# Kernel tuning notes

Hardware: AMD Instinct MI355X
Metric: run time of the kernel (lower is better)

The kernel has to match this reference:

```python
import math
import jax, jax.numpy as jnp
import numpy as np

DIM = 4096
N_HEADS = 32
N_KV_HEADS = 8
HEAD_DIM = DIM // N_HEADS          # 128
N_REP = N_HEADS // N_KV_HEADS      # 4
BATCH = 2
SEQLEN = 2048
MAX_BATCH = 2
MAX_SEQ = 2048
THETA = 10000.0


def _precompute_freqs(dim, end, theta=THETA):
    freqs = 1.0 / theta ** (np.arange(0, dim, 2)[: dim // 2].astype(np.float32) / dim)
    t = np.arange(end, dtype=np.float32)
    ang = np.outer(t, freqs)  # [end, dim//2]
    return jnp.asarray(np.cos(ang), jnp.float32), jnp.asarray(np.sin(ang), jnp.float32)


def setup_inputs() -> dict:
    key = jax.random.key(0)
    ks = jax.random.split(key, 6)
    x = jax.random.normal(ks[0], (BATCH, SEQLEN, DIM), jnp.float32)
    scale = 0.02
    wq = jax.random.normal(ks[1], (DIM, N_HEADS * HEAD_DIM), jnp.float32) * scale
    wk = jax.random.normal(ks[2], (DIM, N_KV_HEADS * HEAD_DIM), jnp.float32) * scale
    wv = jax.random.normal(ks[3], (DIM, N_KV_HEADS * HEAD_DIM), jnp.float32) * scale
    wo = jax.random.normal(ks[4], (N_HEADS * HEAD_DIM, DIM), jnp.float32) * scale
    cache_k = jnp.zeros((MAX_BATCH, MAX_SEQ, N_KV_HEADS, HEAD_DIM), jnp.float32)
    cache_v = jnp.zeros((MAX_BATCH, MAX_SEQ, N_KV_HEADS, HEAD_DIM), jnp.float32)
    freqs_cos, freqs_sin = _precompute_freqs(HEAD_DIM, SEQLEN)
    # additive causal mask, [S, S]
    mask = jnp.where(jnp.tril(jnp.ones((SEQLEN, SEQLEN), bool)), 0.0, -1e9).astype(jnp.float32)
    return {"x": x, "wq": wq, "wk": wk, "wv": wv, "wo": wo,
            "cache_k": cache_k, "cache_v": cache_v,
            "freqs_cos": freqs_cos, "freqs_sin": freqs_sin,
            "mask": mask, "start_pos": 0}


def _apply_rotary(t, cos, sin):
    # t: [B, S, H, D]; cos/sin: [S, D/2] -> broadcast [1, S, 1, D/2]
    B, S, H, D = t.shape
    tr = t.reshape(B, S, H, D // 2, 2)
    re, im = tr[..., 0], tr[..., 1]
    c = cos[None, :, None, :]
    s = sin[None, :, None, :]
    out = jnp.stack([re * c - im * s, re * s + im * c], axis=-1)
    return out.reshape(B, S, H, D)


def reference(x, wq, wk, wv, wo, cache_k, cache_v, freqs_cos, freqs_sin, mask, start_pos):
    B, S, D = x.shape
    xq = (x @ wq).reshape(B, S, N_HEADS, HEAD_DIM)
    xk = (x @ wk).reshape(B, S, N_KV_HEADS, HEAD_DIM)
    xv = (x @ wv).reshape(B, S, N_KV_HEADS, HEAD_DIM)
    xq = _apply_rotary(xq, freqs_cos, freqs_sin)
    xk = _apply_rotary(xk, freqs_cos, freqs_sin)
    # KV-cache write (start_pos is a static Python int)
    ck = cache_k.at[:B, start_pos:start_pos + S].set(xk)
    cv = cache_v.at[:B, start_pos:start_pos + S].set(xv)
    keys = ck[:B, :start_pos + S]    # [B, T, KVH, D]
    values = cv[:B, :start_pos + S]
    # GQA: repeat kv heads
    keys = jnp.repeat(keys, N_REP, axis=2)      # [B, T, H, D]
    values = jnp.repeat(values, N_REP, axis=2)
    scores = jnp.einsum('bqhd,bkhd->bhqk', xq, keys) / math.sqrt(HEAD_DIM)
    scores = scores + mask[None, None, :, :]
    probs = jax.nn.softmax(scores.astype(jnp.float32), axis=-1).astype(xq.dtype)
    out = jnp.einsum('bhqk,bkhd->bqhd', probs, values).reshape(B, S, N_HEADS * HEAD_DIM)
    return out @ wo
```

## Files before the change

### kernel.cpp

```cpp
#include <hip/hip_runtime.h>
#include <stdint.h>

typedef __attribute__((ext_vector_type(4))) float f32x4;
typedef __attribute__((ext_vector_type(4))) unsigned short u16x4;
typedef __attribute__((ext_vector_type(8))) unsigned short u16x8;
typedef __attribute__((ext_vector_type(8))) short s16x8;

#define NH   32
#define NKV  8
#define HD   128
#define SEQ  2048
#define MTOK 4096

__device__ __forceinline__ float b2f(unsigned short u) {
  union { float f; unsigned int i; } v; v.i = ((unsigned int)u) << 16; return v.f;
}
__device__ __forceinline__ unsigned short f2b(float f) {
  unsigned int i = __float_as_uint(f);
  return (unsigned short)((i + 0x7fffu + ((i >> 16) & 1u)) >> 16);
}

__global__ void convert_f32_bf16(const float* __restrict__ in,
                                 unsigned short* __restrict__ out, int n4) {
  int i = blockIdx.x * 256 + threadIdx.x;
  if (i >= n4) return;
  f32x4 v = *(const f32x4*)(in + (size_t)i * 4);
  u16x4 r;
  r.x = f2b(v.x); r.y = f2b(v.y); r.z = f2b(v.z); r.w = f2b(v.w);
  *(u16x4*)(out + (size_t)i * 4) = r;
}

__global__ void tconv(const float* __restrict__ W, unsigned short* __restrict__ WT, int N) {
  __shared__ float tile[32][33];
  int k0 = blockIdx.x * 32, n0 = blockIdx.y * 32;
  int t = threadIdx.x;
  int r = t >> 3;
  int c = (t & 7) * 4;
  f32x4 v = *(const f32x4*)&W[(size_t)(k0 + r) * N + n0 + c];
  tile[r][c + 0] = v.x; tile[r][c + 1] = v.y; tile[r][c + 2] = v.z; tile[r][c + 3] = v.w;
  __syncthreads();
  u16x4 o;
  o.x = f2b(tile[c + 0][r]); o.y = f2b(tile[c + 1][r]);
  o.z = f2b(tile[c + 2][r]); o.w = f2b(tile[c + 3][r]);
  *(u16x4*)&WT[(size_t)(n0 + r) * 4096 + k0 + c] = o;
}

__global__ void vtrans(const unsigned short* __restrict__ vb, unsigned short* __restrict__ vtb) {
  __shared__ unsigned short tile[32][36];
  int s0 = blockIdx.x * 32, d0 = blockIdx.y * 32;
  int bkv = blockIdx.z; int b = bkv >> 3, kvh = bkv & 7;
  int t = threadIdx.x;
  int r = t >> 3, c = (t & 7) * 4;
  u16x4 v = *(const u16x4*)&vb[((size_t)(b * SEQ + s0 + r) * NKV + kvh) * HD + d0 + c];
  tile[r][c + 0] = v.x; tile[r][c + 1] = v.y; tile[r][c + 2] = v.z; tile[r][c + 3] = v.w;
  __syncthreads();
  u16x4 o;
  o.x = tile[c + 0][r]; o.y = tile[c + 1][r]; o.z = tile[c + 2][r]; o.w = tile[c + 3][r];
  *(u16x4*)&vtb[((size_t)(b * NKV + kvh) * HD + d0 + r) * SEQ + s0 + c] = o;
}

__global__ void rope_k(unsigned short* __restrict__ x, const float* __restrict__ cs,
                       const float* __restrict__ sn, int nhShift, int total) {
  int i = blockIdx.x * 256 + threadIdx.x;
  if (i >= total) return;
  int g = i & 15;
  int rem = i >> 4;
  int h = rem & ((1 << nhShift) - 1);
  int sb = rem >> nhShift;
  int s = sb & (SEQ - 1);
  size_t base = (((size_t)sb << nhShift) + h) * HD + g * 8;
  u16x8 v = *(u16x8*)(x + base);
  f32x4 c = *(const f32x4*)(cs + s * 64 + g * 4);
  f32x4 sv = *(const f32x4*)(sn + s * 64 + g * 4);
#pragma unroll
  for (int j = 0; j < 4; ++j) {
    float re = b2f(v[2 * j]), im = b2f(v[2 * j + 1]);
    float cj = c[j], sj = sv[j];
    v[2 * j]     = f2b(re * cj - im * sj);
    v[2 * j + 1] = f2b(re * sj + im * cj);
  }
  *(u16x8*)(x + base) = v;
}

template <typename OutT>
__global__ __launch_bounds__(256, 2)
void gemm_bt(const unsigned short* __restrict__ A, const unsigned short* __restrict__ BT,
             OutT* __restrict__ C, int M, int N, int K) {
  __shared__ __align__(16) unsigned short As[128 * 64];
  __shared__ __align__(16) unsigned short Bs[128 * 64];
  const int t = threadIdx.x;
  const int lane = t & 63;
  const int w = t >> 6;
  const int l15 = lane & 15, l4 = lane >> 4;
  const int wm = w >> 1, wn = w & 1;
  const int m0 = blockIdx.x * 128, n0 = blockIdx.y * 128;

  f32x4 acc[4][4];
#pragma unroll
  for (int i = 0; i < 4; ++i)
#pragma unroll
    for (int j = 0; j < 4; ++j) acc[i][j] = (f32x4)(0.0f);

  for (int k0 = 0; k0 < K; k0 += 64) {
#pragma unroll
    for (int p = 0; p < 4; ++p) {
      int cb = p * 256 + w * 64;
      int c = cb + lane;
      int row = c >> 3, co = (c & 7) * 8;
      const unsigned short* srcA = A + (size_t)(m0 + row) * K + k0 + co;
      const unsigned short* srcB = BT + (size_t)(n0 + row) * K + k0 + co;
      __builtin_amdgcn_global_load_lds((const __attribute__((address_space(1))) void*)srcA,
                                       (__attribute__((address_space(3))) void*)(As + cb * 8),
                                       16, 0, 0);
      __builtin_amdgcn_global_load_lds((const __attribute__((address_space(1))) void*)srcB,
                                       (__attribute__((address_space(3))) void*)(Bs + cb * 8),
                                       16, 0, 0);
    }
    __syncthreads();
    s16x8 af[4][2], bfr[4][2];
#pragma unroll
    for (int mi = 0; mi < 4; ++mi)
#pragma unroll
      for (int kk = 0; kk < 2; ++kk)
        af[mi][kk] = *(const s16x8*)&As[(wm * 64 + mi * 16 + l15) * 64 + kk * 32 + l4 * 8];
#pragma unroll
    for (int ni = 0; ni < 4; ++ni)
#pragma unroll
      for (int kk = 0; kk < 2; ++kk)
        bfr[ni][kk] = *(const s16x8*)&Bs[(wn * 64 + ni * 16 + l15) * 64 + kk * 32 + l4 * 8];
#pragma unroll
    for (int kk = 0; kk < 2; ++kk)
#pragma unroll
      for (int mi = 0; mi < 4; ++mi)
#pragma unroll
        for (int ni = 0; ni < 4; ++ni)
          acc[mi][ni] = __builtin_amdgcn_mfma_f32_16x16x32_bf16(af[mi][kk], bfr[ni][kk],
                                                                acc[mi][ni], 0, 0, 0);
    __syncthreads();
  }
#pragma unroll
  for (int mi = 0; mi < 4; ++mi)
#pragma unroll
    for (int ni = 0; ni < 4; ++ni) {
      int col = n0 + wn * 64 + ni * 16 + l15;
#pragma unroll
      for (int r = 0; r < 4; ++r) {
        int row = m0 + wm * 64 + mi * 16 + l4 * 4 + r;
        if constexpr (sizeof(OutT) == 2)
          C[(size_t)row * N + col] = f2b(acc[mi][ni][r]);
        else
          C[(size_t)row * N + col] = acc[mi][ni][r];
      }
    }
}

template <typename OutT>
__global__ __launch_bounds__(512, 2)
void gemm256(const unsigned short* __restrict__ A, const unsigned short* __restrict__ BT,
             OutT* __restrict__ C, int M, int N, int K) {
  __shared__ __align__(16) unsigned short As[2][256 * 64];
  __shared__ __align__(16) unsigned short Bs[2][256 * 64];
  const int t = threadIdx.x;
  const int lane = t & 63, w = t >> 6;
  const int l15 = lane & 15, l4 = lane >> 4;
  const int wr = w >> 2, wc = w & 3;
  const int m0 = blockIdx.x * 256, n0 = blockIdx.y * 256;
  const int xk = l15 & 7;

  f32x4 acc[8][4];
#pragma unroll
  for (int i = 0; i < 8; ++i)
#pragma unroll
    for (int j = 0; j < 4; ++j) acc[i][j] = (f32x4)(0.0f);

  auto stage = [&](int buf, int k0) {
#pragma unroll
    for (int p = 0; p < 4; ++p) {
      int e = p * 4096 + t * 8;
      int r = e >> 6;
      int bb = (e >> 3) & 7;
      int sc = (bb ^ (r & 7)) << 3;
      int cb = p * 4096 + w * 512;
      __builtin_amdgcn_global_load_lds(
          (const __attribute__((address_space(1))) void*)(A + (size_t)(m0 + r) * K + k0 + sc),
          (__attribute__((address_space(3))) void*)(&As[buf][cb]), 16, 0, 0);
      __builtin_amdgcn_global_load_lds(
          (const __attribute__((address_space(1))) void*)(BT + (size_t)(n0 + r) * K + k0 + sc),
          (__attribute__((address_space(3))) void*)(&Bs[buf][cb]), 16, 0, 0);
    }
  };

  const int NT = K >> 6;
  stage(0, 0);
  asm volatile("s_waitcnt vmcnt(0)" ::: "memory");
  __builtin_amdgcn_s_barrier();
  __builtin_amdgcn_sched_barrier(0);

  for (int kt = 0; kt < NT; ++kt) {
    const int buf = kt & 1;
    if (kt + 1 < NT) {
      stage(buf ^ 1, (kt + 1) * 64);
      asm volatile("s_waitcnt vmcnt(8)" ::: "memory");
    } else {
      asm volatile("s_waitcnt vmcnt(0)" ::: "memory");
    }
    __builtin_amdgcn_s_barrier();
    __builtin_amdgcn_sched_barrier(0);

#pragma unroll
    for (int kk = 0; kk < 2; ++kk) {
      s16x8 af[8], bfr[4];
#pragma unroll
      for (int mi = 0; mi < 8; ++mi) {
        int R = wr * 128 + mi * 16 + l15;
        af[mi] = *(const s16x8*)&As[buf][R * 64 + (((kk * 4 + l4) ^ xk) << 3)];
      }
#pragma unroll
      for (int ni = 0; ni < 4; ++ni) {
        int R = wc * 64 + ni * 16 + l15;
        bfr[ni] = *(const s16x8*)&Bs[buf][R * 64 + (((kk * 4 + l4) ^ xk) << 3)];
      }
      __builtin_amdgcn_s_setprio(1);
#pragma unroll
      for (int mi = 0; mi < 8; ++mi)
#pragma unroll
        for (int ni = 0; ni < 4; ++ni)
          acc[mi][ni] = __builtin_amdgcn_mfma_f32_16x16x32_bf16(af[mi], bfr[ni],
                                                                acc[mi][ni], 0, 0, 0);
      __builtin_amdgcn_s_setprio(0);
    }
    __builtin_amdgcn_s_barrier();
    __builtin_amdgcn_sched_barrier(0);
  }

#pragma unroll
  for (int mi = 0; mi < 8; ++mi)
#pragma unroll
    for (int ni = 0; ni < 4; ++ni) {
      int col = n0 + wc * 64 + ni * 16 + l15;
      int rowb = m0 + wr * 128 + mi * 16 + l4 * 4;
#pragma unroll
      for (int r = 0; r < 4; ++r) {
        if constexpr (sizeof(OutT) == 2)
          C[(size_t)(rowb + r) * N + col] = f2b(acc[mi][ni][r]);
        else
          C[(size_t)(rowb + r) * N + col] = acc[mi][ni][r];
      }
    }
}

__global__ __launch_bounds__(256, 2)
void attn_kernel(const unsigned short* __restrict__ qb, const unsigned short* __restrict__ kb,
                 const unsigned short* __restrict__ vtb, unsigned short* __restrict__ ab) {
  __shared__ __align__(16) unsigned short Ks[64 * 136];
  __shared__ __align__(16) unsigned short Vs[128 * 72];
  __shared__ __align__(16) unsigned short Ps[4 * 16 * 72];
  const int bx = (int)blockIdx.x;
  const int qt = 31 - (bx >> 6);
  const int hb = bx & 63;
  const int h = hb >> 1;
  const int b = hb & 1;
  const int kvh = h >> 2;
  const int t = threadIdx.x, lane = t & 63, w = t >> 6;
  const int l15 = lane & 15, l4 = lane >> 4;
  const int q0 = qt * 64;
  const float SCALE = 0.08838834764831845f;

  size_t qoff = ((size_t)(b * SEQ + q0 + w * 16 + l15) * NH + h) * HD;
  s16x8 qf[4];
#pragma unroll
  for (int kk = 0; kk < 4; ++kk) qf[kk] = *(const s16x8*)(qb + qoff + kk * 32 + l4 * 8);

  f32x4 accO[8];
#pragma unroll
  for (int n = 0; n < 8; ++n) accO[n] = (f32x4)(0.0f);
  float mrow[4] = {-1e30f, -1e30f, -1e30f, -1e30f};
  float lrow[4] = {0.f, 0.f, 0.f, 0.f};
  unsigned short* Pw = Ps + w * 16 * 72;

  u16x8 kreg[4], vreg[4];
  auto load_tile = [&](int k0) {
#pragma unroll
    for (int p = 0; p < 4; ++p) {
      int c = p * 256 + t;
      int krow = c >> 4, kco = (c & 15) * 8;
      kreg[p] = *(const u16x8*)(kb + ((size_t)(b * SEQ + k0 + krow) * NKV + kvh) * HD + kco);
      int vrow = c >> 3, vco = (c & 7) * 8;
      vreg[p] = *(const u16x8*)(vtb + ((size_t)(b * NKV + kvh) * HD + vrow) * SEQ + k0 + vco);
    }
  };
  auto write_tile = [&]() {
#pragma unroll
    for (int p = 0; p < 4; ++p) {
      int c = p * 256 + t;
      *(u16x8*)&Ks[(c >> 4) * 136 + (c & 15) * 8] = kreg[p];
      *(u16x8*)&Vs[(c >> 3) * 72 + (c & 7) * 8] = vreg[p];
    }
  };

  load_tile(0);
  write_tile();
  __syncthreads();

  for (int kt = 0; kt <= qt; ++kt) {
    f32x4 sc[4];
#pragma unroll
    for (int g = 0; g < 4; ++g) sc[g] = (f32x4)(0.0f);
    __builtin_amdgcn_s_setprio(1);
#pragma unroll
    for (int g = 0; g < 4; ++g)
#pragma unroll
      for (int kk = 0; kk < 4; ++kk) {
        s16x8 kf = *(const s16x8*)&Ks[(g * 16 + l15) * 136 + kk * 32 + l4 * 8];
        sc[g] = __builtin_amdgcn_mfma_f32_16x16x32_bf16(qf[kk], kf, sc[g], 0, 0, 0);
      }
    __builtin_amdgcn_s_setprio(0);

    if (kt < qt) load_tile((kt + 1) * 64);

    if (kt == qt) {
#pragma unroll
      for (int g = 0; g < 4; ++g)
#pragma unroll
        for (int r = 0; r < 4; ++r) {
          int key = g * 16 + l15;
          int qr = w * 16 + l4 * 4 + r;
          float v = sc[g][r] * SCALE;
          sc[g][r] = (key <= qr) ? v : -1e30f;
        }
    } else {
#pragma unroll
      for (int g = 0; g < 4; ++g)
#pragma unroll
        for (int r = 0; r < 4; ++r) sc[g][r] *= SCALE;
    }
    float resc[4], newm[4];
#pragma unroll
    for (int r = 0; r < 4; ++r) {
      float tm = fmaxf(fmaxf(sc[0][r], sc[1][r]), fmaxf(sc[2][r], sc[3][r]));
      tm = fmaxf(tm, __shfl_xor(tm, 1));
      tm = fmaxf(tm, __shfl_xor(tm, 2));
      tm = fmaxf(tm, __shfl_xor(tm, 4));
      tm = fmaxf(tm, __shfl_xor(tm, 8));
      newm[r] = fmaxf(mrow[r], tm);
      resc[r] = __expf(mrow[r] - newm[r]);
      mrow[r] = newm[r];
    }
    float pv[4][4];
#pragma unroll
    for (int g = 0; g < 4; ++g)
#pragma unroll
      for (int r = 0; r < 4; ++r) pv[g][r] = __expf(sc[g][r] - newm[r]);
#pragma unroll
    for (int r = 0; r < 4; ++r) {
      float s = pv[0][r] + pv[1][r] + pv[2][r] + pv[3][r];
      s += __shfl_xor(s, 1);
      s += __shfl_xor(s, 2);
      s += __shfl_xor(s, 4);
      s += __shfl_xor(s, 8);
      lrow[r] = lrow[r] * resc[r] + s;
    }
#pragma unroll
    for (int g = 0; g < 4; ++g)
#pragma unroll
      for (int r = 0; r < 4; ++r) Pw[(l4 * 4 + r) * 72 + g * 16 + l15] = f2b(pv[g][r]);
#pragma unroll
    for (int n = 0; n < 8; ++n)
#pragma unroll
      for (int r = 0; r < 4; ++r) accO[n][r] *= resc[r];
    s16x8 pf[2];
    pf[0] = *(const s16x8*)&Pw[l15 * 72 + l4 * 8];
    pf[1] = *(const s16x8*)&Pw[l15 * 72 + 32 + l4 * 8];
    __builtin_amdgcn_s_setprio(1);
#pragma unroll
    for (int n = 0; n < 8; ++n)
#pragma unroll
      for (int kk = 0; kk < 2; ++kk) {
        s16x8 vf = *(const s16x8*)&Vs[(n * 16 + l15) * 72 + kk * 32 + l4 * 8];
        accO[n] = __builtin_amdgcn_mfma_f32_16x16x32_bf16(pf[kk], vf, accO[n], 0, 0, 0);
      }
    __builtin_amdgcn_s_setprio(0);

    __syncthreads();
    if (kt < qt) {
      write_tile();
      __syncthreads();
    }
  }
  float inv[4];
#pragma unroll
  for (int r = 0; r < 4; ++r) inv[r] = 1.0f / lrow[r];
#pragma unroll
  for (int n = 0; n < 8; ++n)
#pragma unroll
    for (int r = 0; r < 4; ++r) {
      int s = q0 + w * 16 + l4 * 4 + r;
      ab[((size_t)(b * SEQ + s) * NH + h) * HD + n * 16 + l15] = f2b(accO[n][r] * inv[r]);
    }
}

extern "C" void kernel_launch(void* const* d_in, const int* in_sizes, int n_in,
                              void* d_out, int out_size, void* d_ws, size_t ws_size,
                              hipStream_t stream) {
  const float* x = (const float*)d_in[0];
  const float* wq = (const float*)d_in[1];
  const float* wk = (const float*)d_in[2];
  const float* wv = (const float*)d_in[3];
  const float* wo = (const float*)d_in[4];
  const float* fcos = (const float*)d_in[7];
  const float* fsin = (const float*)d_in[8];
  float* out = (float*)d_out;

  unsigned short* ws = (unsigned short*)d_ws;
  unsigned short* xb  = ws;
  unsigned short* wqT = ws + 16777216;
  unsigned short* wkT = ws + 33554432;
  unsigned short* wvT = ws + 37748736;
  unsigned short* woT = ws + 41943040;
  unsigned short* qb  = ws + 58720256;
  unsigned short* kb  = ws + 75497472;
  unsigned short* vb  = ws + 79691776;
  unsigned short* vtb = ws + 83886080;
  unsigned short* ab  = ws + 88080384;

  convert_f32_bf16<<<(4194304 + 255) / 256, 256, 0, stream>>>(x, xb, 4194304);
  tconv<<<dim3(128, 128), 256, 0, stream>>>(wq, wqT, 4096);
  tconv<<<dim3(128, 32), 256, 0, stream>>>(wk, wkT, 1024);
  tconv<<<dim3(128, 32), 256, 0, stream>>>(wv, wvT, 1024);
  tconv<<<dim3(128, 128), 256, 0, stream>>>(wo, woT, 4096);

  gemm256<unsigned short><<<dim3(16, 16), 512, 0, stream>>>(xb, wqT, qb, MTOK, 4096, 4096);
  gemm_bt<unsigned short><<<dim3(32, 8), 256, 0, stream>>>(xb, wkT, kb, MTOK, 1024, 4096);
  gemm_bt<unsigned short><<<dim3(32, 8), 256, 0, stream>>>(xb, wvT, vb, MTOK, 1024, 4096);

  rope_k<<<(2097152 + 255) / 256, 256, 0, stream>>>(qb, fcos, fsin, 5, 2097152);
  rope_k<<<(524288 + 255) / 256, 256, 0, stream>>>(kb, fcos, fsin, 3, 524288);

  vtrans<<<dim3(64, 4, 16), 256, 0, stream>>>(vb, vtb);

  attn_kernel<<<2048, 256, 0, stream>>>(qb, kb, vtb, ab);

  gemm256<float><<<dim3(16, 16), 512, 0, stream>>>(ab, woT, out, MTOK, 4096, 4096);
}
```

Before: 932.8 us.

## Fuse K/V projections, swizzle GEMM tiles, add lazy softmax rescale

Computes K and V projections in one GEMM by relying on wkT and wvT being contiguous, giving a combined N=2048 output with K and V interleaved per row. The rope, vtrans and attention kernels are updated to the new stride. gemm256 remaps block indices for better L2 locality and moves the barrier inside the kk loop with an explicit lgkmcnt wait. Attention now rescales the running max and accumulators only when some row max grows by more than 8, which skips most exp and multiply work but can let unnormalised values grow.

```diff
diff --git a/kernel.cpp b/kernel.cpp
--- a/kernel.cpp
+++ b/kernel.cpp
@@ -45,13 +45,13 @@
   *(u16x4*)&WT[(size_t)(n0 + r) * 4096 + k0 + c] = o;
 }
 
-__global__ void vtrans(const unsigned short* __restrict__ vb, unsigned short* __restrict__ vtb) {
+__global__ void vtrans(const unsigned short* __restrict__ kvb, unsigned short* __restrict__ vtb) {
   __shared__ unsigned short tile[32][36];
   int s0 = blockIdx.x * 32, d0 = blockIdx.y * 32;
   int bkv = blockIdx.z; int b = bkv >> 3, kvh = bkv & 7;
   int t = threadIdx.x;
   int r = t >> 3, c = (t & 7) * 4;
-  u16x4 v = *(const u16x4*)&vb[((size_t)(b * SEQ + s0 + r) * NKV + kvh) * HD + d0 + c];
+  u16x4 v = *(const u16x4*)&kvb[(size_t)(b * SEQ + s0 + r) * 2048 + 1024 + kvh * HD + d0 + c];
   tile[r][c + 0] = v.x; tile[r][c + 1] = v.y; tile[r][c + 2] = v.z; tile[r][c + 3] = v.w;
   __syncthreads();
   u16x4 o;
@@ -82,6 +82,29 @@
   *(u16x8*)(x + base) = v;
 }
 
+__global__ void rope_kv(unsigned short* __restrict__ kvb, const float* __restrict__ cs,
+                        const float* __restrict__ sn, int total) {
+  int i = blockIdx.x * 256 + threadIdx.x;
+  if (i >= total) return;
+  int g = i & 15;
+  int rem = i >> 4;
+  int h = rem & 7;
+  int sb = rem >> 3;
+  int s = sb & (SEQ - 1);
+  size_t base = (size_t)sb * 2048 + h * HD + g * 8;
+  u16x8 v = *(u16x8*)(kvb + base);
+  f32x4 c = *(const f32x4*)(cs + s * 64 + g * 4);
+  f32x4 sv = *(const f32x4*)(sn + s * 64 + g * 4);
+#pragma unroll
+  for (int j = 0; j < 4; ++j) {
+    float re = b2f(v[2 * j]), im = b2f(v[2 * j + 1]);
+    float cj = c[j], sj = sv[j];
+    v[2 * j]     = f2b(re * cj - im * sj);
+    v[2 * j + 1] = f2b(re * sj + im * cj);
+  }
+  *(u16x8*)(kvb + base) = v;
+}
+
 template <typename OutT>
 __global__ __launch_bounds__(256, 2)
 void gemm_bt(const unsigned short* __restrict__ A, const unsigned short* __restrict__ BT,
@@ -164,7 +187,9 @@
   const int lane = t & 63, w = t >> 6;
   const int l15 = lane & 15, l4 = lane >> 4;
   const int wr = w >> 2, wc = w & 3;
-  const int m0 = blockIdx.x * 256, n0 = blockIdx.y * 256;
+  const int flat = (int)blockIdx.x + 16 * (int)blockIdx.y;
+  const int f2 = (flat & 7) * 32 + (flat >> 3);
+  const int m0 = (f2 & 15) * 256, n0 = (f2 >> 4) * 256;
   const int xk = l15 & 7;
 
   f32x4 acc[8][4];
@@ -220,6 +245,8 @@
         int R = wc * 64 + ni * 16 + l15;
         bfr[ni] = *(const s16x8*)&Bs[buf][R * 64 + (((kk * 4 + l4) ^ xk) << 3)];
       }
+      asm volatile("s_waitcnt lgkmcnt(0)" ::: "memory");
+      __builtin_amdgcn_sched_barrier(0);
       __builtin_amdgcn_s_setprio(1);
 #pragma unroll
       for (int mi = 0; mi < 8; ++mi)
@@ -228,9 +255,9 @@
           acc[mi][ni] = __builtin_amdgcn_mfma_f32_16x16x32_bf16(af[mi], bfr[ni],
                                                                 acc[mi][ni], 0, 0, 0);
       __builtin_amdgcn_s_setprio(0);
-    }
-    __builtin_amdgcn_s_barrier();
-    __builtin_amdgcn_sched_barrier(0);
+      __builtin_amdgcn_s_barrier();
+      __builtin_amdgcn_sched_barrier(0);
+    }
   }
 
 #pragma unroll
@@ -250,7 +277,7 @@
 }
 
 __global__ __launch_bounds__(256, 2)
-void attn_kernel(const unsigned short* __restrict__ qb, const unsigned short* __restrict__ kb,
+void attn_kernel(const unsigned short* __restrict__ qb, const unsigned short* __restrict__ kvb,
                  const unsigned short* __restrict__ vtb, unsigned short* __restrict__ ab) {
   __shared__ __align__(16) unsigned short Ks[64 * 136];
   __shared__ __align__(16) unsigned short Vs[128 * 72];
@@ -284,7 +311,7 @@
     for (int p = 0; p < 4; ++p) {
       int c = p * 256 + t;
       int krow = c >> 4, kco = (c & 15) * 8;
-      kreg[p] = *(const u16x8*)(kb + ((size_t)(b * SEQ + k0 + krow) * NKV + kvh) * HD + kco);
+      kreg[p] = *(const u16x8*)(kvb + (size_t)(b * SEQ + k0 + krow) * 2048 + kvh * HD + kco);
       int vrow = c >> 3, vco = (c & 7) * 8;
       vreg[p] = *(const u16x8*)(vtb + ((size_t)(b * NKV + kvh) * HD + vrow) * SEQ + k0 + vco);
     }
@@ -334,23 +361,34 @@
 #pragma unroll
         for (int r = 0; r < 4; ++r) sc[g][r] *= SCALE;
     }
-    float resc[4], newm[4];
+    float tm[4];
 #pragma unroll
     for (int r = 0; r < 4; ++r) {
-      float tm = fmaxf(fmaxf(sc[0][r], sc[1][r]), fmaxf(sc[2][r], sc[3][r]));
-      tm = fmaxf(tm, __shfl_xor(tm, 1));
-      tm = fmaxf(tm, __shfl_xor(tm, 2));
-      tm = fmaxf(tm, __shfl_xor(tm, 4));
-      tm = fmaxf(tm, __shfl_xor(tm, 8));
-      newm[r] = fmaxf(mrow[r], tm);
-      resc[r] = __expf(mrow[r] - newm[r]);
-      mrow[r] = newm[r];
+      float v = fmaxf(fmaxf(sc[0][r], sc[1][r]), fmaxf(sc[2][r], sc[3][r]));
+      v = fmaxf(v, __shfl_xor(v, 1));
+      v = fmaxf(v, __shfl_xor(v, 2));
+      v = fmaxf(v, __shfl_xor(v, 4));
+      v = fmaxf(v, __shfl_xor(v, 8));
+      tm[r] = v;
+    }
+    bool grow = (tm[0] > mrow[0] + 8.f) || (tm[1] > mrow[1] + 8.f) ||
+                (tm[2] > mrow[2] + 8.f) || (tm[3] > mrow[3] + 8.f);
+    if (__any(grow)) {
+#pragma unroll
+      for (int r = 0; r < 4; ++r) {
+        float nm = fmaxf(mrow[r], tm[r]);
+        float rs = __expf(mrow[r] - nm);
+        mrow[r] = nm;
+        lrow[r] *= rs;
+#pragma unroll
+        for (int n = 0; n < 8; ++n) accO[n][r] *= rs;
+      }
     }
     float pv[4][4];
 #pragma unroll
     for (int g = 0; g < 4; ++g)
 #pragma unroll
-      for (int r = 0; r < 4; ++r) pv[g][r] = __expf(sc[g][r] - newm[r]);
+      for (int r = 0; r < 4; ++r) pv[g][r] = __expf(sc[g][r] - mrow[r]);
 #pragma unroll
     for (int r = 0; r < 4; ++r) {
       float s = pv[0][r] + pv[1][r] + pv[2][r] + pv[3][r];
@@ -358,16 +396,12 @@
       s += __shfl_xor(s, 2);
       s += __shfl_xor(s, 4);
       s += __shfl_xor(s, 8);
-      lrow[r] = lrow[r] * resc[r] + s;
+      lrow[r] += s;
     }
 #pragma unroll
     for (int g = 0; g < 4; ++g)
 #pragma unroll
       for (int r = 0; r < 4; ++r) Pw[(l4 * 4 + r) * 72 + g * 16 + l15] = f2b(pv[g][r]);
-#pragma unroll
-    for (int n = 0; n < 8; ++n)
-#pragma unroll
-      for (int r = 0; r < 4; ++r) accO[n][r] *= resc[r];
     s16x8 pf[2];
     pf[0] = *(const s16x8*)&Pw[l15 * 72 + l4 * 8];
     pf[1] = *(const s16x8*)&Pw[l15 * 72 + 32 + l4 * 8];
@@ -418,8 +452,7 @@
   unsigned short* wvT = ws + 37748736;
   unsigned short* woT = ws + 41943040;
   unsigned short* qb  = ws + 58720256;
-  unsigned short* kb  = ws + 75497472;
-  unsigned short* vb  = ws + 79691776;
+  unsigned short* kvb = ws + 75497472;
   unsigned short* vtb = ws + 83886080;
   unsigned short* ab  = ws + 88080384;
 
@@ -430,15 +463,14 @@
   tconv<<<dim3(128, 128), 256, 0, stream>>>(wo, woT, 4096);
 
   gemm256<unsigned short><<<dim3(16, 16), 512, 0, stream>>>(xb, wqT, qb, MTOK, 4096, 4096);
-  gemm_bt<unsigned short><<<dim3(32, 8), 256, 0, stream>>>(xb, wkT, kb, MTOK, 1024, 4096);
-  gemm_bt<unsigned short><<<dim3(32, 8), 256, 0, stream>>>(xb, wvT, vb, MTOK, 1024, 4096);
+  gemm_bt<unsigned short><<<dim3(32, 16), 256, 0, stream>>>(xb, wkT, kvb, MTOK, 2048, 4096);
 
   rope_k<<<(2097152 + 255) / 256, 256, 0, stream>>>(qb, fcos, fsin, 5, 2097152);
-  rope_k<<<(524288 + 255) / 256, 256, 0, stream>>>(kb, fcos, fsin, 3, 524288);
-
-  vtrans<<<dim3(64, 4, 16), 256, 0, stream>>>(vb, vtb);
-
-  attn_kernel<<<2048, 256, 0, stream>>>(qb, kb, vtb, ab);
+  rope_kv<<<(524288 + 255) / 256, 256, 0, stream>>>(kvb, fcos, fsin, 524288);
+
+  vtrans<<<dim3(64, 4, 16), 256, 0, stream>>>(kvb, vtb);
+
+  attn_kernel<<<2048, 256, 0, stream>>>(qb, kvb, vtb, ab);
 
   gemm256<float><<<dim3(16, 16), 512, 0, stream>>>(ab, woT, out, MTOK, 4096, 4096);
 }
```

Result: faster. 903.9 us (-3.1%).
